# Optimization experiments

Hardware: AMD Instinct MI355X
Metric: run time of the kernel (lower is better)

The kernel has to match this reference:

```python
import jax, jax.numpy as jnp
import numpy as np

N = 10000
E = 320000
IN = 10000
HID = 128
NCLS = 2


def setup_inputs() -> dict:
    key = jax.random.key(0)
    ks = jax.random.split(key, 8)
    x = jax.random.normal(ks[0], (N, IN), dtype=jnp.float32)
    edge_index = jax.random.randint(ks[1], (2, E), 0, N, dtype=jnp.int64)
    edge_weight = jax.random.uniform(ks[2], (E,), dtype=jnp.float32)
    # GCNConv linear (no bias folding issues: PyG GCNConv uses Linear(in, out, bias=False) + separate bias)
    W_conv = jax.random.normal(ks[3], (IN, HID), dtype=jnp.float32) / np.sqrt(IN)
    b_conv = jnp.zeros((HID,), dtype=jnp.float32)
    W_lin = jax.random.normal(ks[4], (HID, NCLS), dtype=jnp.float32) / np.sqrt(HID)
    b_lin = jnp.zeros((NCLS,), dtype=jnp.float32)
    return {"x": x, "edge_index": edge_index, "edge_weight": edge_weight,
            "W_conv": W_conv, "b_conv": b_conv, "W_lin": W_lin, "b_lin": b_lin}


def reference(x, edge_index, edge_weight, W_conv, b_conv, W_lin, b_lin):
    n = x.shape[0]
    row, col = edge_index[0], edge_index[1]
    # add self loops with weight 1 (GCNConv add_self_loops=True, fill_value=1.)
    loop = jnp.arange(n, dtype=row.dtype)
    row = jnp.concatenate([row, loop])
    col = jnp.concatenate([col, loop])
    ew = jnp.concatenate([edge_weight, jnp.ones((n,), dtype=edge_weight.dtype)])
    # symmetric GCN normalization: deg from destination (col) index
    deg = jax.ops.segment_sum(ew, col, num_segments=n)
    dinv = jnp.where(deg > 0, jax.lax.rsqrt(deg), 0.0)
    norm = dinv[row] * ew * dinv[col]  # [E+N]
    # linear transform then weighted scatter-add aggregation
    h = x @ W_conv                      # [N, HID]
    msg = norm[:, None] * h[row]        # [E+N, HID] gather on source nodes
    out = jax.ops.segment_sum(msg, col, num_segments=n) + b_conv  # [N, HID]
    out = jax.nn.relu(out)
    # dropout p=0.0 is identity
    logits = out @ W_lin + b_lin        # [N, 2]
    return jax.nn.softmax(logits, axis=1)
```

## Files before the change

kernel.cpp:

```cpp
#include <hip/hip_runtime.h>
#include <hip/hip_bf16.h>
#include <math.h>

#define NN   10000
#define NE   320000
#define KK   10000
#define HID  128
#define KPAD 10048
#define MT   79
#define KITERS 157
#define NSPLIT 8

typedef __bf16 bf16x8 __attribute__((ext_vector_type(8)));
typedef float  f32x16 __attribute__((ext_vector_type(16)));

#define OFF_DINV 0u
#define OFF_FLAG 40960u
#define OFF_ER   65536u
#define OFF_EC   1572864u
#define OFF_H    3145728u
#define OFF_AGG  8388608u
#define OFF_WT   13631488u

__device__ inline unsigned short f2bf(float f) {
  unsigned int v = __builtin_bit_cast(unsigned int, f);
  unsigned int lsb = (v >> 16) & 1u;
  v += 0x7fffu + lsb;
  return (unsigned short)(v >> 16);
}

__global__ __launch_bounds__(64) void k_detect(const int* __restrict__ ei,
                                               int* __restrict__ flag) {
  int t = threadIdx.x;
  int v = ei[2*t + 1];
  unsigned long long b = __ballot(v != 0);
  if (t == 0) flag[0] = (b == 0ull) ? 1 : 0;
}

__global__ __launch_bounds__(256) void k_edges(const int* __restrict__ ei,
                                               const int* __restrict__ flag,
                                               int* __restrict__ er,
                                               int* __restrict__ ec) {
  int e = blockIdx.x*256 + threadIdx.x;
  if (e < NE) {
    int s = flag[0];
    er[e] = ei[(size_t)e << s];
    ec[e] = ei[((size_t)(NE + e)) << s];
  }
}

__global__ __launch_bounds__(256) void k_transpose(const float* __restrict__ W,
                                                   unsigned short* __restrict__ Wt) {
  __shared__ float t[32][33];
  const int tx = threadIdx.x, ty = threadIdx.y;
  const int bk = blockIdx.x, bn = blockIdx.y;
#pragma unroll
  for (int j = 0; j < 4; ++j) {
    int k = bk*32 + ty + j*8;
    int n = bn*32 + tx;
    float v = 0.0f;
    if (k < KK) v = W[(size_t)k*HID + n];
    t[ty + j*8][tx] = v;
  }
  __syncthreads();
#pragma unroll
  for (int j = 0; j < 4; ++j) {
    int n = bn*32 + ty + j*8;
    int k = bk*32 + tx;
    Wt[(size_t)n*KPAD + k] = f2bf(t[tx][ty + j*8]);
  }
}

__global__ __launch_bounds__(256) void k_deg(const int* __restrict__ ec,
                                             const float* __restrict__ ew,
                                             float* __restrict__ deg) {
  int e = blockIdx.x*256 + threadIdx.x;
  if (e < NE) atomicAdd(&deg[ec[e]], ew[e]);
}

__global__ __launch_bounds__(256) void k_dinv(float* __restrict__ deg) {
  int i = blockIdx.x*256 + threadIdx.x;
  if (i < NN) {
    float d = deg[i] + 1.0f;
    deg[i] = (d > 0.0f) ? (1.0f / sqrtf(d)) : 0.0f;
  }
}

__global__ __launch_bounds__(256) void k_gemm(const float* __restrict__ xg,
                                              const unsigned short* __restrict__ Wt,
                                              float* __restrict__ h) {
  __shared__ unsigned short lA[128*64];
  __shared__ unsigned short lB[128*64];
  const int tid  = threadIdx.x;
  const int lane = tid & 63;
  const int w    = tid >> 6;
  const int bid  = blockIdx.x;
  const int mt   = bid % MT;
  const int kc   = bid / MT;
  const int m0   = mt * 128;
  const int it0  = (KITERS * kc) / NSPLIT;
  const int it1  = (KITERS * (kc + 1)) / NSPLIT;

  const int srow = tid >> 3;
  const int scol = (tid & 7) * 8;
  const float* pA[4];
  const unsigned short* pB[4];
#pragma unroll
  for (int r = 0; r < 4; ++r) {
    int ga = m0 + r*32 + srow; if (ga > NN-1) ga = NN-1;
    pA[r] = xg + (size_t)ga * KK + scol;
    pB[r] = Wt + (size_t)(r*32 + srow) * KPAD + scol;
  }

  f32x16 acc[4];
#pragma unroll
  for (int ct = 0; ct < 4; ++ct)
#pragma unroll
    for (int q = 0; q < 16; ++q) acc[ct][q] = 0.0f;

  for (int it = it0; it < it1; ++it) {
    const int k0 = it * 64;
    __syncthreads();
#pragma unroll
    for (int r = 0; r < 4; ++r) {
      __builtin_amdgcn_global_load_lds(
          (const __attribute__((address_space(1))) unsigned int*)(pB[r] + k0),
          (__attribute__((address_space(3))) unsigned int*)(&lB[r*2048 + tid*8]),
          16, 0, 0);
    }
#pragma unroll
    for (int r = 0; r < 4; ++r) {
      float4 f0 = make_float4(0.f,0.f,0.f,0.f), f1 = f0;
      if ((k0 + scol) < KK) {
        f0 = *(const float4*)(pA[r] + k0);
        f1 = *(const float4*)(pA[r] + k0 + 4);
      }
      uint4 u;
      u.x = (unsigned)f2bf(f0.x) | ((unsigned)f2bf(f0.y) << 16);
      u.y = (unsigned)f2bf(f0.z) | ((unsigned)f2bf(f0.w) << 16);
      u.z = (unsigned)f2bf(f1.x) | ((unsigned)f2bf(f1.y) << 16);
      u.w = (unsigned)f2bf(f1.z) | ((unsigned)f2bf(f1.w) << 16);
      *((uint4*)&lA[r*2048 + tid*8]) = u;
    }
    __syncthreads();

    const unsigned short* Arow = &lA[(w*32 + (lane & 31))*64 + (lane >> 5)*8];
    const unsigned short* Brow = &lB[((lane & 31))*64 + (lane >> 5)*8];
#pragma unroll
    for (int s = 0; s < 4; ++s) {
      bf16x8 a = *(const bf16x8*)(Arow + s*16);
#pragma unroll
      for (int ct = 0; ct < 4; ++ct) {
        bf16x8 b = *(const bf16x8*)(Brow + ct*2048 + s*16);
        acc[ct] = __builtin_amdgcn_mfma_f32_32x32x16_bf16(a, b, acc[ct], 0, 0, 0);
      }
    }
  }

#pragma unroll
  for (int ct = 0; ct < 4; ++ct) {
    int col = ct*32 + (lane & 31);
#pragma unroll
    for (int reg = 0; reg < 16; ++reg) {
      int rloc = (reg & 3) + 8*(reg >> 2) + 4*(lane >> 5);
      int row = m0 + w*32 + rloc;
      if (row < NN) atomicAdd(&h[(size_t)row*HID + col], acc[ct][reg]);
    }
  }
}

__global__ __launch_bounds__(256) void k_agg(const int* __restrict__ er,
                                             const int* __restrict__ ec,
                                             const float* __restrict__ ew,
                                             const float* __restrict__ dinv,
                                             const float* __restrict__ h,
                                             float* __restrict__ agg) {
  int e = blockIdx.x*4 + (threadIdx.x >> 6);
  if (e >= NE) return;
  int lane = threadIdx.x & 63;
  int r = er[e], c = ec[e];
  float nrm = dinv[r] * ew[e] * dinv[c];
  float v0 = nrm * h[(size_t)r*HID + lane];
  float v1 = nrm * h[(size_t)r*HID + 64 + lane];
  atomicAdd(&agg[(size_t)c*HID + lane],      v0);
  atomicAdd(&agg[(size_t)c*HID + 64 + lane], v1);
}

__global__ __launch_bounds__(256) void k_out(const float* __restrict__ agg,
                                             const float* __restrict__ h,
                                             const float* __restrict__ dinv,
                                             const float* __restrict__ bc,
                                             const float* __restrict__ Wl,
                                             const float* __restrict__ bl,
                                             float* __restrict__ out) {
  int i = blockIdx.x*4 + (threadIdx.x >> 6);
  if (i >= NN) return;
  int lane = threadIdx.x & 63;
  float di = dinv[i], d2 = di*di;
  float v0 = agg[(size_t)i*HID + lane]      + d2*h[(size_t)i*HID + lane]      + bc[lane];
  float v1 = agg[(size_t)i*HID + 64 + lane] + d2*h[(size_t)i*HID + 64 + lane] + bc[64+lane];
  v0 = fmaxf(v0, 0.0f); v1 = fmaxf(v1, 0.0f);
  float l0 = v0*Wl[lane*2]     + v1*Wl[(64+lane)*2];
  float l1 = v0*Wl[lane*2 + 1] + v1*Wl[(64+lane)*2 + 1];
#pragma unroll
  for (int off = 32; off > 0; off >>= 1) {
    l0 += __shfl_down(l0, off);
    l1 += __shfl_down(l1, off);
  }
  if (lane == 0) {
    l0 += bl[0]; l1 += bl[1];
    float m  = fmaxf(l0, l1);
    float e0 = expf(l0 - m), e1 = expf(l1 - m);
    float s  = 1.0f / (e0 + e1);
    *(float2*)(out + (size_t)i*2) = make_float2(e0 * s, e1 * s);
  }
}

extern "C" void kernel_launch(void* const* d_in, const int* in_sizes, int n_in,
                              void* d_out, int out_size, void* d_ws, size_t ws_size,
                              hipStream_t stream) {
  (void)in_sizes; (void)n_in; (void)out_size; (void)ws_size;
  const float* x  = (const float*)d_in[0];
  const int*   ei = (const int*)d_in[1];
  const float* ew = (const float*)d_in[2];
  const float* Wc = (const float*)d_in[3];
  const float* bc = (const float*)d_in[4];
  const float* Wl = (const float*)d_in[5];
  const float* bl = (const float*)d_in[6];

  char* ws = (char*)d_ws;
  float* dinv = (float*)(ws + OFF_DINV);
  int*   flag = (int*)(ws + OFF_FLAG);
  int*   er   = (int*)(ws + OFF_ER);
  int*   ec   = (int*)(ws + OFF_EC);
  float* h    = (float*)(ws + OFF_H);
  float* agg  = (float*)(ws + OFF_AGG);
  unsigned short* Wt = (unsigned short*)(ws + OFF_WT);
  float* out = (float*)d_out;

  hipMemsetAsync(dinv, 0, NN*sizeof(float), stream);
  hipMemsetAsync(h,    0, (size_t)NN*HID*sizeof(float), stream);
  hipMemsetAsync(agg,  0, (size_t)NN*HID*sizeof(float), stream);

  k_detect<<<1, 64, 0, stream>>>(ei, flag);
  k_edges <<<(NE + 255)/256, 256, 0, stream>>>(ei, flag, er, ec);
  k_transpose<<<dim3(KPAD/32, HID/32), dim3(32, 8), 0, stream>>>(Wc, Wt);
  k_deg <<<(NE + 255)/256, 256, 0, stream>>>(ec, ew, dinv);
  k_dinv<<<(NN + 255)/256, 256, 0, stream>>>(dinv);
  k_gemm<<<MT*NSPLIT, 256, 0, stream>>>(x, Wt, h);
  k_agg <<<NE/4, 256, 0, stream>>>(er, ec, ew, dinv, h, agg);
  k_out <<<NN/4, 256, 0, stream>>>(agg, h, dinv, bc, Wl, bl, out);
}
```

Baseline: 743.8 us.

## Replace atomic scatter aggregation with CSR gather fused into output kernel

Builds a destination-sorted CSR (count, scan, atomic-cursor scatter with precomputed normalized weights) and replaces the per-edge atomicAdd scatter into an agg buffer with a per-node gather loop. The gather is fused with the bias/relu/linear/softmax output kernel, which removes the agg buffer, its memset and its re-read. The cost is extra small kernels: a single-block serial scan and a scatter pass that uses atomics on a cursor array. Edge order within each node becomes nondeterministic, so the floating-point summation order can vary between runs.

```diff
diff --git a/kernel.cpp b/kernel.cpp
--- a/kernel.cpp
+++ b/kernel.cpp
@@ -16,10 +16,14 @@
 
 #define OFF_DINV 0u
 #define OFF_FLAG 40960u
-#define OFF_ER   65536u
+#define OFF_CNT  45056u
+#define OFF_ROW  86016u
+#define OFF_CUR  126976u
+#define OFF_ER   262144u
 #define OFF_EC   1572864u
-#define OFF_H    3145728u
-#define OFF_AGG  8388608u
+#define OFF_CSRS 2883584u
+#define OFF_CSRW 4194304u
+#define OFF_H    8388608u
 #define OFF_WT   13631488u
 
 __device__ inline unsigned short f2bf(float f) {
@@ -73,9 +77,14 @@
 
 __global__ __launch_bounds__(256) void k_deg(const int* __restrict__ ec,
                                              const float* __restrict__ ew,
-                                             float* __restrict__ deg) {
+                                             float* __restrict__ deg,
+                                             int* __restrict__ cnt) {
   int e = blockIdx.x*256 + threadIdx.x;
-  if (e < NE) atomicAdd(&deg[ec[e]], ew[e]);
+  if (e < NE) {
+    int c = ec[e];
+    atomicAdd(&deg[c], ew[e]);
+    atomicAdd(&cnt[c], 1);
+  }
 }
 
 __global__ __launch_bounds__(256) void k_dinv(float* __restrict__ deg) {
@@ -83,6 +92,54 @@
   if (i < NN) {
     float d = deg[i] + 1.0f;
     deg[i] = (d > 0.0f) ? (1.0f / sqrtf(d)) : 0.0f;
+  }
+}
+
+__global__ __launch_bounds__(256) void k_scan(const int* __restrict__ cnt,
+                                              int* __restrict__ rowstart,
+                                              int* __restrict__ cursor) {
+  __shared__ int sums[256];
+  const int t = threadIdx.x;
+  const int CH = 40;
+  const int base = t * CH;
+  int s = 0;
+  for (int k = 0; k < CH; ++k) {
+    int i = base + k;
+    if (i < NN) s += cnt[i];
+  }
+  sums[t] = s;
+  __syncthreads();
+  for (int off = 1; off < 256; off <<= 1) {
+    int add = (t >= off) ? sums[t - off] : 0;
+    __syncthreads();
+    sums[t] += add;
+    __syncthreads();
+  }
+  int run = (t == 0) ? 0 : sums[t - 1];
+  for (int k = 0; k < CH; ++k) {
+    int i = base + k;
+    if (i < NN) {
+      rowstart[i] = run;
+      cursor[i]   = run;
+      run += cnt[i];
+    }
+  }
+  if (t == 255) rowstart[NN] = run;
+}
+
+__global__ __launch_bounds__(256) void k_scatter(const int* __restrict__ er,
+                                                 const int* __restrict__ ec,
+                                                 const float* __restrict__ ew,
+                                                 const float* __restrict__ dinv,
+                                                 int* __restrict__ cursor,
+                                                 int* __restrict__ csr_src,
+                                                 float* __restrict__ csr_w) {
+  int e = blockIdx.x*256 + threadIdx.x;
+  if (e < NE) {
+    int r = er[e], c = ec[e];
+    int slot = atomicAdd(&cursor[c], 1);
+    csr_src[slot] = r;
+    csr_w[slot]   = dinv[r] * ew[e] * dinv[c];
   }
 }
 
@@ -169,39 +226,49 @@
   }
 }
 
-__global__ __launch_bounds__(256) void k_agg(const int* __restrict__ er,
-                                             const int* __restrict__ ec,
-                                             const float* __restrict__ ew,
-                                             const float* __restrict__ dinv,
-                                             const float* __restrict__ h,
-                                             float* __restrict__ agg) {
-  int e = blockIdx.x*4 + (threadIdx.x >> 6);
-  if (e >= NE) return;
-  int lane = threadIdx.x & 63;
-  int r = er[e], c = ec[e];
-  float nrm = dinv[r] * ew[e] * dinv[c];
-  float v0 = nrm * h[(size_t)r*HID + lane];
-  float v1 = nrm * h[(size_t)r*HID + 64 + lane];
-  atomicAdd(&agg[(size_t)c*HID + lane],      v0);
-  atomicAdd(&agg[(size_t)c*HID + 64 + lane], v1);
-}
-
-__global__ __launch_bounds__(256) void k_out(const float* __restrict__ agg,
-                                             const float* __restrict__ h,
-                                             const float* __restrict__ dinv,
-                                             const float* __restrict__ bc,
-                                             const float* __restrict__ Wl,
-                                             const float* __restrict__ bl,
-                                             float* __restrict__ out) {
+__global__ __launch_bounds__(256) void k_aggout(const int* __restrict__ rowstart,
+                                                const int* __restrict__ csr_src,
+                                                const float* __restrict__ csr_w,
+                                                const float* __restrict__ h,
+                                                const float* __restrict__ dinv,
+                                                const float* __restrict__ bc,
+                                                const float* __restrict__ Wl,
+                                                const float* __restrict__ bl,
+                                                float* __restrict__ out) {
   int i = blockIdx.x*4 + (threadIdx.x >> 6);
   if (i >= NN) return;
   int lane = threadIdx.x & 63;
+  const float* hp = h + 2*lane;
+  int j  = rowstart[i];
+  int j1 = rowstart[i + 1];
+
+  float ax = 0.f, ay = 0.f;
+  for (; j + 3 < j1; j += 4) {
+    int   s0 = csr_src[j],   s1 = csr_src[j+1], s2 = csr_src[j+2], s3 = csr_src[j+3];
+    float w0 = csr_w[j],     w1 = csr_w[j+1],   w2 = csr_w[j+2],   w3 = csr_w[j+3];
+    float2 a = *(const float2*)(hp + (size_t)s0*HID);
+    float2 b = *(const float2*)(hp + (size_t)s1*HID);
+    float2 c = *(const float2*)(hp + (size_t)s2*HID);
+    float2 d = *(const float2*)(hp + (size_t)s3*HID);
+    ax += w0*a.x + w1*b.x + w2*c.x + w3*d.x;
+    ay += w0*a.y + w1*b.y + w2*c.y + w3*d.y;
+  }
+  for (; j < j1; ++j) {
+    int   s0 = csr_src[j];
+    float w0 = csr_w[j];
+    float2 a = *(const float2*)(hp + (size_t)s0*HID);
+    ax += w0*a.x; ay += w0*a.y;
+  }
+
   float di = dinv[i], d2 = di*di;
-  float v0 = agg[(size_t)i*HID + lane]      + d2*h[(size_t)i*HID + lane]      + bc[lane];
-  float v1 = agg[(size_t)i*HID + 64 + lane] + d2*h[(size_t)i*HID + 64 + lane] + bc[64+lane];
-  v0 = fmaxf(v0, 0.0f); v1 = fmaxf(v1, 0.0f);
-  float l0 = v0*Wl[lane*2]     + v1*Wl[(64+lane)*2];
-  float l1 = v0*Wl[lane*2 + 1] + v1*Wl[(64+lane)*2 + 1];
+  float2 hs = *(const float2*)(hp + (size_t)i*HID);
+  float2 bb = *(const float2*)(bc + 2*lane);
+  float v0 = fmaxf(ax + d2*hs.x + bb.x, 0.0f);
+  float v1 = fmaxf(ay + d2*hs.y + bb.y, 0.0f);
+
+  float4 w4 = *(const float4*)(Wl + 4*lane);
+  float l0 = v0*w4.x + v1*w4.z;
+  float l1 = v0*w4.y + v1*w4.w;
 #pragma unroll
   for (int off = 32; off > 0; off >>= 1) {
     l0 += __shfl_down(l0, off);
@@ -231,23 +298,28 @@
   char* ws = (char*)d_ws;
   float* dinv = (float*)(ws + OFF_DINV);
   int*   flag = (int*)(ws + OFF_FLAG);
+  int*   cnt  = (int*)(ws + OFF_CNT);
+  int*   row  = (int*)(ws + OFF_ROW);
+  int*   cur  = (int*)(ws + OFF_CUR);
   int*   er   = (int*)(ws + OFF_ER);
   int*   ec   = (int*)(ws + OFF_EC);
+  int*   csrs = (int*)(ws + OFF_CSRS);
+  float* csrw = (float*)(ws + OFF_CSRW);
   float* h    = (float*)(ws + OFF_H);
-  float* agg  = (float*)(ws + OFF_AGG);
   unsigned short* Wt = (unsigned short*)(ws + OFF_WT);
   float* out = (float*)d_out;
 
   hipMemsetAsync(dinv, 0, NN*sizeof(float), stream);
+  hipMemsetAsync(cnt,  0, NN*sizeof(int),   stream);
   hipMemsetAsync(h,    0, (size_t)NN*HID*sizeof(float), stream);
-  hipMemsetAsync(agg,  0, (size_t)NN*HID*sizeof(float), stream);
 
   k_detect<<<1, 64, 0, stream>>>(ei, flag);
   k_edges <<<(NE + 255)/256, 256, 0, stream>>>(ei, flag, er, ec);
   k_transpose<<<dim3(KPAD/32, HID/32), dim3(32, 8), 0, stream>>>(Wc, Wt);
-  k_deg <<<(NE + 255)/256, 256, 0, stream>>>(ec, ew, dinv);
+  k_deg <<<(NE + 255)/256, 256, 0, stream>>>(ec, ew, dinv, cnt);
   k_dinv<<<(NN + 255)/256, 256, 0, stream>>>(dinv);
+  k_scan<<<1, 256, 0, stream>>>(cnt, row, cur);
+  k_scatter<<<(NE + 255)/256, 256, 0, stream>>>(er, ec, ew, dinv, cur, csrs, csrw);
   k_gemm<<<MT*NSPLIT, 256, 0, stream>>>(x, Wt, h);
-  k_agg <<<NE/4, 256, 0, stream>>>(er, ec, ew, dinv, h, agg);
-  k_out <<<NN/4, 256, 0, stream>>>(agg, h, dinv, bc, Wl, bl, out);
-}
+  k_aggout<<<NN/4, 256, 0, stream>>>(row, csrs, csrw, h, dinv, bc, Wl, bl, out);
+}
```

Result: faster. 692.3 us (-6.9%).
